# Performance work log

Hardware: AMD Instinct MI355X
Metric: run time of the kernel (lower is better)

## Reference

```python
import jax, jax.numpy as jnp
import numpy as np

RES = (256, 256)
FLOW_TEMP_REG = 1e-3
LOSS_SCALING = True
EPS = 1e-9


def get_interpolation(events, flow, tref, res):
    # events: [B,N,4] (ts,y,x,p); flow: [B,N,2] per-event (flow_y, flow_x)
    warped = events[:, :, 1:3] + (tref - events[:, :, 0:1]) * flow  # [B,N,2] (y,x)
    top_y = jnp.floor(warped[:, :, 0:1])
    bot_y = top_y + 1.0
    left_x = jnp.floor(warped[:, :, 1:2])
    right_x = left_x + 1.0
    # four bilinear corners stacked along the event dim -> [B,4N,2]
    idx = jnp.concatenate([
        jnp.concatenate([top_y, left_x], axis=2),
        jnp.concatenate([top_y, right_x], axis=2),
        jnp.concatenate([bot_y, left_x], axis=2),
        jnp.concatenate([bot_y, right_x], axis=2)], axis=1)
    w = jnp.maximum(0.0, 1.0 - jnp.abs(jnp.tile(warped, (1, 4, 1)) - idx))  # [B,4N,2]
    mask = ((idx[:, :, 0:1] >= 0) & (idx[:, :, 0:1] < res[0]) &
            (idx[:, :, 1:2] >= 0) & (idx[:, :, 1:2] < res[1])).astype(w.dtype)
    idx = idx * mask  # out-of-bounds -> pixel 0 with zero weight
    w = w * mask
    flat_idx = (idx[:, :, 0] * res[1] + idx[:, :, 1]).astype(jnp.int32)  # [B,4N]
    weights = w[:, :, 0] * w[:, :, 1]  # bilinear weight, [B,4N]
    return flat_idx, weights


def interpolate(flat_idx, w, npix):
    # per-batch scatter-add of weights into a flat pixel grid -> [B, H*W]
    return jax.vmap(lambda i, v: jax.ops.segment_sum(v, i, num_segments=npix))(flat_idx, w)


def scale_loss(iwe_pos, iwe_neg, iwe_pos_ts, iwe_neg_ts):
    loss = jnp.sum(iwe_pos_ts ** 2, axis=1) + jnp.sum(iwe_neg_ts ** 2, axis=1)  # [B]
    if LOSS_SCALING:
        nonzero_px = jnp.sum(((iwe_pos + iwe_neg) != 0).astype(loss.dtype), axis=1)
        loss = loss / (nonzero_px + EPS)
    return jnp.sum(loss)


def forward(event_list, flow, pol_mask, vector_list, max_ts):
    res = RES
    npix = res[0] * res[1]
    mt = jnp.asarray(max_ts, jnp.float32)
    pm = jnp.tile(pol_mask, (1, 4, 1))                    # [B,4N,2]
    ts4 = jnp.tile(event_list[:, :, 0], (1, 4))           # [B,4N]
    loss = jnp.float32(0.0)
    # forward warp (tref=max_ts, weight ts) and backward warp (tref=0, weight max_ts-ts)
    for tref, ts_w in ((mt, ts4), (jnp.float32(0.0), mt - ts4)):
        idx, w = get_interpolation(event_list, flow, tref, res)
        wp = w * pm[:, :, 0]
        wn = w * pm[:, :, 1]
        iwe_pos = interpolate(idx, wp, npix)
        iwe_neg = interpolate(idx, wn, npix)
        iwe_pos_ts = interpolate(idx, wp * ts_w, npix) / (iwe_pos + EPS) / mt
        iwe_neg_ts = interpolate(idx, wn * ts_w, npix) / (iwe_neg + EPS) / mt
        loss = loss + scale_loss(iwe_pos, iwe_neg, iwe_pos_ts, iwe_neg_ts)
    # single flow scale in _flow_list -> divide by 1
    loss = loss / 1.0
    # Charbonnier temporal smoothness on flow vectors [B,P,8]
    dt = vector_list[:, :-1, :] - vector_list[:, 1:, :]
    dt = jnp.sqrt(dt ** 2 + EPS).reshape(vector_list.shape[0], -1)
    loss = loss + FLOW_TEMP_REG * jnp.sum(jnp.mean(dt, axis=1))
    return loss


def setup_inputs() -> dict:
    B, N, P = 8, 262144, 4
    H, W = RES
    key = jax.random.key(0)
    ks = jax.random.split(key, 6)
    ts = jax.random.uniform(ks[0], (B, N, 1), dtype=jnp.float32) * P
    y = jax.random.uniform(ks[1], (B, N, 1), dtype=jnp.float32) * (H - 1)
    x = jax.random.uniform(ks[2], (B, N, 1), dtype=jnp.float32) * (W - 1)
    p = jax.random.bernoulli(ks[3], 0.5, (B, N, 1)).astype(jnp.float32) * 2.0 - 1.0
    event_list = jnp.concatenate([ts, y, x, p], axis=2)
    pos = (p > 0).astype(jnp.float32)
    pol_mask = jnp.concatenate([pos, 1.0 - pos], axis=2)
    flow = jax.random.normal(ks[4], (B, N, 2), dtype=jnp.float32) * 2.0
    vector_list = jax.random.normal(ks[5], (B, P, 8), dtype=jnp.float32)
    return {"event_list": event_list, "flow": flow, "pol_mask": pol_mask,
            "vector_list": vector_list, "max_ts": P}


def reference(event_list, flow, pol_mask, vector_list, max_ts):
    return forward(event_list, flow, pol_mask, vector_list, max_ts)
```

## Files before the change

kernel.cpp:

```cpp
#include <hip/hip_runtime.h>
#include <math.h>

#define RES_H 256
#define RES_W 256
#define NPIX 65536
#define EPSF 1e-9f
#define FLOW_TEMP_REG 1e-3f

#define BAND_SHIFT 3
#define BAND_ROWS 8
#define N_BANDS 32
#define BAND_PX (BAND_ROWS * RES_W)
#define NBUCKET 64
#define CAP 16384
#define QS 2048.0f
#define QINV (1.0f / 2048.0f)
#define EV_PER_BLOCK 1024
#define EV_PER_THREAD 4

#define PAD 32

typedef unsigned long long u64;
typedef unsigned int u32;


__device__ __forceinline__ float decode_mt(const int* p) {
    int raw = *p;
    if (raw >= 0 && raw < (1 << 23)) return (float)raw;
    union { int i; float f; } u; u.i = raw; return u.f;
}


__global__ void __launch_bounds__(256, 8) ew_bin(
    const float4* __restrict__ ev, const float2* __restrict__ flow,
    const int* __restrict__ mt_ptr, u64* __restrict__ recs,
    u32* __restrict__ counts, int N)
{
    __shared__ u32 hist[NBUCKET], basebuf[NBUCKET], cursor[NBUCKET];
    const int b = blockIdx.y;
    const int start = blockIdx.x * EV_PER_BLOCK;
    const int tid = threadIdx.x;
    if (tid < NBUCKET) { hist[tid] = 0u; cursor[tid] = 0u; }
    __syncthreads();

    const float mt = decode_mt(mt_ptr);
    const float inv_mt = 1.0f / mt;

    float4 e[EV_PER_THREAD];
    float2 f[EV_PER_THREAD];
    #pragma unroll
    for (int j = 0; j < EV_PER_THREAD; ++j) {
        int i = start + tid + j * 256;
        if (i < N) { e[j] = ev[b * N + i]; f[j] = flow[b * N + i]; }
        else { e[j] = make_float4(0.f, -100.f, -100.f, 1.f); f[j] = make_float2(0.f, 0.f); }
    }

    #pragma unroll
    for (int j = 0; j < EV_PER_THREAD; ++j) {
        #pragma unroll
        for (int dir = 0; dir < 2; ++dir) {
            float dtt = (dir ? 0.0f : mt) - e[j].x;
            float wy = fminf(fmaxf(e[j].y + dtt * f[j].x, -8.0f), 264.0f);
            float wx = fminf(fmaxf(e[j].z + dtt * f[j].y, -8.0f), 264.0f);
            int wyf = __float2int_rn(wy * 4096.0f);
            int wxf = __float2int_rn(wx * 4096.0f);
            int iy = wyf >> 12, ix = wxf >> 12;
            if (iy < -1 || iy > 255 || ix < -1 || ix > 255) continue;
            int t1 = iy >> BAND_SHIFT;
            int t2 = (iy + 1) >> BAND_SHIFT;
            if (t1 >= 0) atomicAdd(&hist[dir * N_BANDS + t1], 1u);
            if (t2 <= N_BANDS - 1 && t2 != t1) atomicAdd(&hist[dir * N_BANDS + t2], 1u);
        }
    }
    __syncthreads();
    if (tid < NBUCKET) basebuf[tid] = atomicAdd(&counts[(b * NBUCKET + tid) * PAD], hist[tid]);
    __syncthreads();

    #pragma unroll
    for (int j = 0; j < EV_PER_THREAD; ++j) {
        #pragma unroll
        for (int dir = 0; dir < 2; ++dir) {
            float dtt = (dir ? 0.0f : mt) - e[j].x;
            float tswn = (dir ? (mt - e[j].x) : e[j].x) * inv_mt;
            float wy = fminf(fmaxf(e[j].y + dtt * f[j].x, -8.0f), 264.0f);
            float wx = fminf(fmaxf(e[j].z + dtt * f[j].y, -8.0f), 264.0f);
            int wyf = __float2int_rn(wy * 4096.0f);
            int wxf = __float2int_rn(wx * 4096.0f);
            int iy = wyf >> 12, ix = wxf >> 12;
            if (iy < -1 || iy > 255 || ix < -1 || ix > 255) continue;
            u32 tq = __float2uint_rn(fminf(fmaxf(tswn, 0.0f), 1.0f) * 4096.0f);
            u64 rec = (u64)((u32)wyf & 0x3FFFFFu)
                    | ((u64)((u32)wxf & 0x3FFFFFu) << 22)
                    | ((u64)tq << 44)
                    | ((u64)(e[j].w > 0.0f ? 0u : 1u) << 57);
            int t1 = iy >> BAND_SHIFT;
            int t2 = (iy + 1) >> BAND_SHIFT;
            #pragma unroll
            for (int s = 0; s < 2; ++s) {
                int t = s ? t2 : t1;
                if (t < 0 || t > N_BANDS - 1) continue;
                if (s && t2 == t1) continue;
                int k = dir * N_BANDS + t;
                u32 off = atomicAdd(&cursor[k], 1u);
                u32 slot = basebuf[k] + off;
                if (slot >= CAP) slot = CAP - 1;
                recs[(size_t)(b * NBUCKET + k) * CAP + slot] = rec;
            }
        }
    }
}

__global__ void __launch_bounds__(1024, 8) ew_accum(
    const u64* __restrict__ recs, const u32* __restrict__ counts,
    float* __restrict__ partials)
{
    __shared__ u32 lds[2 * BAND_PX];
    __shared__ float wterm[16], wnz[16];
    const int band = blockIdx.x, bd = blockIdx.y;
    const int q = bd * N_BANDS + band;
    const int row0 = band << BAND_SHIFT;
    const int tid = threadIdx.x;
    for (int i = tid; i < 2 * BAND_PX; i += 1024) lds[i] = 0u;
    __syncthreads();

    u32 cnt = counts[q * PAD]; if (cnt > CAP) cnt = CAP;
    const u64* bucket = recs + (size_t)q * CAP;

    for (u32 i = tid; i < cnt; i += 1024) {
        u64 rec = bucket[i];
        int wyf = ((int)(((u32)rec & 0x3FFFFFu) << 10)) >> 10;
        int wxf = ((int)(((u32)(rec >> 22) & 0x3FFFFFu) << 10)) >> 10;
        float tswn = (float)((u32)(rec >> 44) & 0x1FFFu) * (1.0f / 4096.0f);
        u32 pol = (u32)(rec >> 57) & 1u;
        int ry = (wyf >> 12) - row0;
        int ix = wxf >> 12;
        float fy = (float)(wyf & 0xFFF) * (1.0f / 4096.0f);
        float fx = (float)(wxf & 0xFFF) * (1.0f / 4096.0f);
        u32* pl = lds + pol * BAND_PX;
        #pragma unroll
        for (int cc = 0; cc < 4; ++cc) {
            int cy = ry + (cc >> 1), cx = ix + (cc & 1);
            if ((unsigned)cy >= BAND_ROWS || (unsigned)cx >= RES_W) continue;
            float wgt = ((cc >> 1) ? fy : 1.0f - fy) * ((cc & 1) ? fx : 1.0f - fx);
            u32 v = (__float2uint_rn(wgt * tswn * QS) << 16)
                  |  __float2uint_rn(wgt * QS);
            if (v) atomicAdd(&pl[(cy << 8) | cx], v);
        }
    }
    __syncthreads();

    const uint2 pp = ((const uint2*)lds)[tid];
    const uint2 nn = ((const uint2*)(lds + BAND_PX))[tid];
    const u32 pu[2] = {pp.x, pp.y};
    const u32 nu[2] = {nn.x, nn.y};
    float term = 0.0f, nz = 0.0f;
    #pragma unroll
    for (int j = 0; j < 2; ++j) {
        u32 wp_r = pu[j] & 0xFFFFu, tp_r = pu[j] >> 16;
        u32 wn_r = nu[j] & 0xFFFFu, tn_r = nu[j] >> 16;
        float wp = (float)wp_r * QINV, tp = (float)tp_r * QINV;
        float wn = (float)wn_r * QINV, tn = (float)tn_r * QINV;
        float pts = tp / (wp + EPSF);
        float nts = tn / (wn + EPSF);
        term += pts * pts + nts * nts;
        nz   += ((wp_r | wn_r) != 0u) ? 1.0f : 0.0f;
    }
    #pragma unroll
    for (int off = 32; off > 0; off >>= 1) {
        term += __shfl_down(term, off);
        nz   += __shfl_down(nz, off);
    }
    if ((tid & 63) == 0) { wterm[tid >> 6] = term; wnz[tid >> 6] = nz; }
    __syncthreads();
    if (tid == 0) {
        float t = 0.0f, z = 0.0f;
        #pragma unroll
        for (int wv = 0; wv < 16; ++wv) { t += wterm[wv]; z += wnz[wv]; }
        atomicAdd(&partials[bd * PAD + 0], t);
        atomicAdd(&partials[bd * PAD + 1], z);
    }
}

__global__ void __launch_bounds__(256) ew_finalize(
    const float* __restrict__ partials, const float* __restrict__ vec,
    float* __restrict__ out, int B, int P, int n_bd)
{
    int tid = threadIdx.x;
    float v = 0.0f;
    if (tid < n_bd) {
        float s = partials[tid * PAD + 0];
        float n = partials[tid * PAD + 1];
        v = s / (n + EPSF);
    }
    int per_b = (P - 1) * 8;
    int total = B * per_b;
    float sm = 0.0f;
    for (int i = tid; i < total; i += blockDim.x) {
        int b = i / per_b;
        int r = i - b * per_b;
        int pi = r >> 3, j = r & 7;
        float d = vec[(b * P + pi) * 8 + j] - vec[(b * P + pi + 1) * 8 + j];
        sm += sqrtf(d * d + EPSF);
    }
    sm = sm / (float)per_b * FLOW_TEMP_REG;

    __shared__ float sdata[256];
    sdata[tid] = v + sm;
    __syncthreads();
    for (int s = 128; s > 0; s >>= 1) {
        if (tid < s) sdata[tid] += sdata[tid + s];
        __syncthreads();
    }
    if (tid == 0) out[0] = sdata[0];
}

extern "C" void kernel_launch(void* const* d_in, const int* in_sizes, int n_in,
                              void* d_out, int out_size, void* d_ws, size_t ws_size,
                              hipStream_t stream) {
    const float4* ev   = (const float4*)d_in[0];
    const float2* flow = (const float2*)d_in[1];
    const float*  vec  = (const float*)d_in[3];
    const int*    mtp  = (const int*)d_in[4];

    const int B = 8;
    const int N = in_sizes[0] / (B * 4);
    const int P = in_sizes[3] / (B * 8);

    u32*   counts   = (u32*)d_ws;
    float* partials = (float*)((char*)d_ws + 65536);
    u64*   recs     = (u64*)((char*)d_ws + 131072);

    hipMemsetAsync(d_ws, 0, 131072, stream);

    dim3 bgrid((N + EV_PER_BLOCK - 1) / EV_PER_BLOCK, B);
    ew_bin<<<bgrid, 256, 0, stream>>>(ev, flow, mtp, recs, counts, N);

    dim3 agrid(N_BANDS, 16);
    ew_accum<<<agrid, 1024, 0, stream>>>(recs, counts, partials);

    ew_finalize<<<1, 256, 0, stream>>>(partials, vec, (float*)d_out, B, P, 16);
}
```

Baseline: 128.8 us.

## Replace global-atomic bucket offsets with fixed per-block slices

The binning kernel no longer makes a histogram pass or reserves space in each bucket with global atomics. Each block now writes its records into a fixed 96-entry slice per bucket and stores a per-block count. The accumulate kernel walks these slices one wave per block slice, which removes the first pass and the global atomic contention. The cost is that any records beyond 96 per block and bucket are silently dropped, and slices that are only partly filled make reads more scattered.

```diff
diff --git a/kernel.cpp b/kernel.cpp
--- a/kernel.cpp
+++ b/kernel.cpp
@@ -12,12 +12,11 @@
 #define N_BANDS 32
 #define BAND_PX (BAND_ROWS * RES_W)
 #define NBUCKET 64
-#define CAP 16384
+#define SLICE 96
 #define QS 2048.0f
 #define QINV (1.0f / 2048.0f)
 #define EV_PER_BLOCK 1024
 #define EV_PER_THREAD 4
-
 #define PAD 32
 
 typedef unsigned long long u64;
@@ -34,13 +33,13 @@
 __global__ void __launch_bounds__(256, 8) ew_bin(
     const float4* __restrict__ ev, const float2* __restrict__ flow,
     const int* __restrict__ mt_ptr, u64* __restrict__ recs,
-    u32* __restrict__ counts, int N)
+    u32* __restrict__ cnts, int N, int nblk)
 {
-    __shared__ u32 hist[NBUCKET], basebuf[NBUCKET], cursor[NBUCKET];
-    const int b = blockIdx.y;
-    const int start = blockIdx.x * EV_PER_BLOCK;
+    __shared__ u32 cursor[NBUCKET];
+    const int b = blockIdx.y, blkx = blockIdx.x;
+    const int start = blkx * EV_PER_BLOCK;
     const int tid = threadIdx.x;
-    if (tid < NBUCKET) { hist[tid] = 0u; cursor[tid] = 0u; }
+    if (tid < NBUCKET) cursor[tid] = 0u;
     __syncthreads();
 
     const float mt = decode_mt(mt_ptr);
@@ -54,27 +53,6 @@
         if (i < N) { e[j] = ev[b * N + i]; f[j] = flow[b * N + i]; }
         else { e[j] = make_float4(0.f, -100.f, -100.f, 1.f); f[j] = make_float2(0.f, 0.f); }
     }
-
-    #pragma unroll
-    for (int j = 0; j < EV_PER_THREAD; ++j) {
-        #pragma unroll
-        for (int dir = 0; dir < 2; ++dir) {
-            float dtt = (dir ? 0.0f : mt) - e[j].x;
-            float wy = fminf(fmaxf(e[j].y + dtt * f[j].x, -8.0f), 264.0f);
-            float wx = fminf(fmaxf(e[j].z + dtt * f[j].y, -8.0f), 264.0f);
-            int wyf = __float2int_rn(wy * 4096.0f);
-            int wxf = __float2int_rn(wx * 4096.0f);
-            int iy = wyf >> 12, ix = wxf >> 12;
-            if (iy < -1 || iy > 255 || ix < -1 || ix > 255) continue;
-            int t1 = iy >> BAND_SHIFT;
-            int t2 = (iy + 1) >> BAND_SHIFT;
-            if (t1 >= 0) atomicAdd(&hist[dir * N_BANDS + t1], 1u);
-            if (t2 <= N_BANDS - 1 && t2 != t1) atomicAdd(&hist[dir * N_BANDS + t2], 1u);
-        }
-    }
-    __syncthreads();
-    if (tid < NBUCKET) basebuf[tid] = atomicAdd(&counts[(b * NBUCKET + tid) * PAD], hist[tid]);
-    __syncthreads();
 
     #pragma unroll
     for (int j = 0; j < EV_PER_THREAD; ++j) {
@@ -102,17 +80,22 @@
                 if (s && t2 == t1) continue;
                 int k = dir * N_BANDS + t;
                 u32 off = atomicAdd(&cursor[k], 1u);
-                u32 slot = basebuf[k] + off;
-                if (slot >= CAP) slot = CAP - 1;
-                recs[(size_t)(b * NBUCKET + k) * CAP + slot] = rec;
+                if (off < SLICE)
+                    recs[((size_t)(b * NBUCKET + k) * nblk + blkx) * SLICE + off] = rec;
             }
         }
     }
-}
-
-__global__ void __launch_bounds__(1024, 8) ew_accum(
-    const u64* __restrict__ recs, const u32* __restrict__ counts,
-    float* __restrict__ partials)
+    __syncthreads();
+
+    if (tid < NBUCKET) {
+        u32 c = cursor[tid];
+        cnts[(size_t)(b * NBUCKET + tid) * nblk + blkx] = (c < SLICE) ? c : SLICE;
+    }
+}
+
+__global__ void __launch_bounds__(1024, 2) ew_accum(
+    const u64* __restrict__ recs, const u32* __restrict__ cnts,
+    float* __restrict__ partials, int nblk)
 {
     __shared__ u32 lds[2 * BAND_PX];
     __shared__ float wterm[16], wnz[16];
@@ -123,28 +106,31 @@
     for (int i = tid; i < 2 * BAND_PX; i += 1024) lds[i] = 0u;
     __syncthreads();
 
-    u32 cnt = counts[q * PAD]; if (cnt > CAP) cnt = CAP;
-    const u64* bucket = recs + (size_t)q * CAP;
-
-    for (u32 i = tid; i < cnt; i += 1024) {
-        u64 rec = bucket[i];
-        int wyf = ((int)(((u32)rec & 0x3FFFFFu) << 10)) >> 10;
-        int wxf = ((int)(((u32)(rec >> 22) & 0x3FFFFFu) << 10)) >> 10;
-        float tswn = (float)((u32)(rec >> 44) & 0x1FFFu) * (1.0f / 4096.0f);
-        u32 pol = (u32)(rec >> 57) & 1u;
-        int ry = (wyf >> 12) - row0;
-        int ix = wxf >> 12;
-        float fy = (float)(wyf & 0xFFF) * (1.0f / 4096.0f);
-        float fx = (float)(wxf & 0xFFF) * (1.0f / 4096.0f);
-        u32* pl = lds + pol * BAND_PX;
-        #pragma unroll
-        for (int cc = 0; cc < 4; ++cc) {
-            int cy = ry + (cc >> 1), cx = ix + (cc & 1);
-            if ((unsigned)cy >= BAND_ROWS || (unsigned)cx >= RES_W) continue;
-            float wgt = ((cc >> 1) ? fy : 1.0f - fy) * ((cc & 1) ? fx : 1.0f - fx);
-            u32 v = (__float2uint_rn(wgt * tswn * QS) << 16)
-                  |  __float2uint_rn(wgt * QS);
-            if (v) atomicAdd(&pl[(cy << 8) | cx], v);
+    const int wave = tid >> 6, lane = tid & 63;
+    for (int blk = wave; blk < nblk; blk += 16) {
+        u32 c = cnts[(size_t)q * nblk + blk];
+        if (c > SLICE) c = SLICE;
+        const u64* sl = recs + ((size_t)q * nblk + blk) * SLICE;
+        for (u32 i = lane; i < c; i += 64) {
+            u64 rec = sl[i];
+            int wyf = ((int)(((u32)rec & 0x3FFFFFu) << 10)) >> 10;
+            int wxf = ((int)(((u32)(rec >> 22) & 0x3FFFFFu) << 10)) >> 10;
+            float tswn = (float)((u32)(rec >> 44) & 0x1FFFu) * (1.0f / 4096.0f);
+            u32 pol = (u32)(rec >> 57) & 1u;
+            int ry = (wyf >> 12) - row0;
+            int ix = wxf >> 12;
+            float fy = (float)(wyf & 0xFFF) * (1.0f / 4096.0f);
+            float fx = (float)(wxf & 0xFFF) * (1.0f / 4096.0f);
+            u32* pl = lds + pol * BAND_PX;
+            #pragma unroll
+            for (int cc = 0; cc < 4; ++cc) {
+                int cy = ry + (cc >> 1), cx = ix + (cc & 1);
+                if ((unsigned)cy >= BAND_ROWS || (unsigned)cx >= RES_W) continue;
+                float wgt = ((cc >> 1) ? fy : 1.0f - fy) * ((cc & 1) ? fx : 1.0f - fx);
+                u32 v = (__float2uint_rn(wgt * tswn * QS) << 16)
+                      |  __float2uint_rn(wgt * QS);
+                if (v) atomicAdd(&pl[(cy << 8) | cx], v);
+            }
         }
     }
     __syncthreads();
@@ -225,18 +211,19 @@
     const int B = 8;
     const int N = in_sizes[0] / (B * 4);
     const int P = in_sizes[3] / (B * 8);
-
-    u32*   counts   = (u32*)d_ws;
-    float* partials = (float*)((char*)d_ws + 65536);
-    u64*   recs     = (u64*)((char*)d_ws + 131072);
-
-    hipMemsetAsync(d_ws, 0, 131072, stream);
-
-    dim3 bgrid((N + EV_PER_BLOCK - 1) / EV_PER_BLOCK, B);
-    ew_bin<<<bgrid, 256, 0, stream>>>(ev, flow, mtp, recs, counts, N);
+    const int nblk = (N + EV_PER_BLOCK - 1) / EV_PER_BLOCK;
+
+    float* partials = (float*)d_ws;
+    u32*   cnts     = (u32*)((char*)d_ws + 65536);
+    u64*   recs     = (u64*)((char*)d_ws + (1 << 20));
+
+    hipMemsetAsync(d_ws, 0, 4096, stream);
+
+    dim3 bgrid(nblk, B);
+    ew_bin<<<bgrid, 256, 0, stream>>>(ev, flow, mtp, recs, cnts, N, nblk);
 
     dim3 agrid(N_BANDS, 16);
-    ew_accum<<<agrid, 1024, 0, stream>>>(recs, counts, partials);
+    ew_accum<<<agrid, 1024, 0, stream>>>(recs, cnts, partials, nblk);
 
     ew_finalize<<<1, 256, 0, stream>>>(partials, vec, (float*)d_out, B, P, 16);
 }
```

New measurement: 143.7 us. +11.5%, slower.
